# Kernel tuning notes

Measured on AMD Instinct MI355X. Metric: run time of the kernel, lower is better.

Reference implementation:

```python
import jax, jax.numpy as jnp
import numpy as np

B, L, D, H = 2, 4, 512, 8
HD = D // H
BLOCK, T_IDX, SEM = 2048, 2047, 50
NUM_VQ, CLIP = 1024, 512
T = T_IDX + 1  # condition token + idx tokens


def _ln(x, g, b):
    m = x.mean(-1, keepdims=True)
    v = ((x - m) ** 2).mean(-1, keepdims=True)
    return (x - m) * jax.lax.rsqrt(v + 1e-5) * g + b


def setup_inputs() -> dict:
    key = jax.random.key(0)
    ks = iter(jax.random.split(key, 48))
    p = lambda shape: 0.02 * jax.random.normal(next(ks), shape, jnp.float32)
    inp = {
        'idx': jax.random.randint(next(ks), (B, T_IDX), 0, NUM_VQ + 2, jnp.int32),
        'clip_feature': jax.random.normal(next(ks), (B, CLIP), jnp.float32),
        'tok_emb0': p((NUM_VQ + 2, D)),
        'tok_emb1': p((NUM_VQ + 2, D)),
        'cond_w': p((CLIP, D)), 'cond_b': jnp.zeros((D,), jnp.float32),
        'pos_emb': p((BLOCK, D)),
        'ln1_g': jnp.ones((L, D), jnp.float32), 'ln1_b': jnp.zeros((L, D), jnp.float32),
        'wq': p((L, D, D)), 'bq': jnp.zeros((L, D), jnp.float32),
        'wk': p((L, D, D)), 'bk': jnp.zeros((L, D), jnp.float32),
        'wv': p((L, D, D)), 'bv': jnp.zeros((L, D), jnp.float32),
        'wo': p((L, D, D)), 'bo': jnp.zeros((L, D), jnp.float32),
        'ln2_g': jnp.ones((L, D), jnp.float32), 'ln2_b': jnp.zeros((L, D), jnp.float32),
        'w1': p((L, D, 4 * D)), 'b1': jnp.zeros((L, 4 * D), jnp.float32),
        'w2': p((L, 4 * D, D)), 'b2': jnp.zeros((L, D), jnp.float32),
    }
    return inp


def reference(idx, clip_feature, tok_emb0, tok_emb1, cond_w, cond_b, pos_emb,
              ln1_g, ln1_b, wq, bq, wk, bk, wv, bv, wo, bo,
              ln2_g, ln2_b, w1, b1, w2, b2):
    # condition embedding + dual token embeddings (semantic / reconstruction split)
    cond = (clip_feature @ cond_w + cond_b)[:, None, :]          # [B,1,D]
    sem = tok_emb0[idx[:, :SEM]]                                  # [B,SEM,D]
    rec = tok_emb1[idx[:, SEM:]]                                  # [B,T_IDX-SEM,D]
    x = jnp.concatenate([cond, sem, rec], axis=1) + pos_emb[None, :T]  # [B,T,D]

    scale = 1.0 / np.sqrt(HD)
    causal = jnp.tril(jnp.ones((T, T), bool))                     # key <= query
    for i in range(L):
        h = _ln(x, ln1_g[i], ln1_b[i])
        q = (h @ wq[i] + bq[i]).reshape(B, T, H, HD)
        k = (h @ wk[i] + bk[i]).reshape(B, T, H, HD)
        v = (h @ wv[i] + bv[i]).reshape(B, T, H, HD)
        att = jnp.einsum('bthd,bshd->bhts', q, k) * scale        # [B,H,T,T]
        att = jnp.where(causal, att, -jnp.inf)
        att = jax.nn.softmax(att, axis=-1)
        y = jnp.einsum('bhts,bshd->bthd', att, v).reshape(B, T, D)
        x = x + y @ wo[i] + bo[i]
        h2 = _ln(x, ln2_g[i], ln2_b[i])
        x = x + jax.nn.gelu(h2 @ w1[i] + b1[i], approximate=False) @ w2[i] + b2[i]
    return x
```

## Files before the change

kernel.cpp:

```cpp
#include <hip/hip_runtime.h>
#include <math.h>

#define BB 2
#define TT 2048
#define DD 512
#define LL 4
#define HH 8
#define HDD 64
#define SEMN 50
#define CLIPN 512
#define NTOK (BB*TT)
#define QS 1024
#define VST 2056

typedef __bf16 bf16x8 __attribute__((ext_vector_type(8)));
typedef __bf16 bf16x4 __attribute__((ext_vector_type(4)));
typedef float  f32x4  __attribute__((ext_vector_type(4)));

#if __has_builtin(__builtin_amdgcn_global_load_lds)
#define USE_GLL 1
#endif

__device__ __forceinline__ void gll16(const __bf16* g, __bf16* l) {
#ifdef USE_GLL
  __builtin_amdgcn_global_load_lds((const __attribute__((address_space(1))) void*)g,
                                   (__attribute__((address_space(3))) void*)l, 16, 0, 0);
#endif
}

__device__ __forceinline__ float fexp2(float x) {
#if __has_builtin(__builtin_amdgcn_exp2f)
  return __builtin_amdgcn_exp2f(x);
#else
  return exp2f(x);
#endif
}

__global__ __launch_bounds__(128) void embed_kernel(
    const int* __restrict__ idx,
    const float* __restrict__ tok0, const float* __restrict__ tok1,
    const float* __restrict__ pos, float* __restrict__ x) {
  int row = blockIdx.x;
  int b = row / TT, t = row % TT;
  if (t == 0) return;
  int d4 = threadIdx.x << 2;
  int tok = idx[b*(TT-1) + (t-1)];
  const float* te = (t <= SEMN) ? tok0 : tok1;
  float4 e = *(const float4*)&te[(size_t)tok*DD + d4];
  float4 p = *(const float4*)&pos[(size_t)t*DD + d4];
  e.x += p.x; e.y += p.y; e.z += p.z; e.w += p.w;
  *(float4*)&x[(size_t)row*DD + d4] = e;
}

__global__ __launch_bounds__(256) void cond_kernel(
    const float* __restrict__ clip, const float* __restrict__ cw,
    const float* __restrict__ cb, const float* __restrict__ pos,
    float* __restrict__ x) {
  __shared__ float4 part[8][32];
  int b = blockIdx.x >> 2, dc = blockIdx.x & 3;
  int tid = threadIdx.x;
  int dv = tid & 31;
  int cg = tid >> 5;
  int d4 = dc*128 + dv*4;
  const float* cr = clip + b*CLIPN + cg*64;
  float4 acc = {0.f, 0.f, 0.f, 0.f};
  #pragma unroll 8
  for (int i = 0; i < 64; ++i) {
    float cv = cr[i];
    float4 w4 = *(const float4*)&cw[(size_t)(cg*64 + i)*DD + d4];
    acc.x = fmaf(cv, w4.x, acc.x); acc.y = fmaf(cv, w4.y, acc.y);
    acc.z = fmaf(cv, w4.z, acc.z); acc.w = fmaf(cv, w4.w, acc.w);
  }
  part[cg][dv] = acc;
  __syncthreads();
  if (tid < 32) {
    int dd4 = dc*128 + tid*4;
    float4 s = part[0][tid];
    #pragma unroll
    for (int g = 1; g < 8; ++g) {
      float4 q = part[g][tid];
      s.x += q.x; s.y += q.y; s.z += q.z; s.w += q.w;
    }
    float4 cbv = *(const float4*)&cb[dd4];
    float4 pv  = *(const float4*)&pos[dd4];
    s.x += cbv.x + pv.x; s.y += cbv.y + pv.y;
    s.z += cbv.z + pv.z; s.w += cbv.w + pv.w;
    *(float4*)&x[(size_t)(b*TT)*DD + dd4] = s;
  }
}

__global__ __launch_bounds__(256) void ln_kernel(const float* __restrict__ x,
                                                 const float* __restrict__ g,
                                                 const float* __restrict__ bta,
                                                 __bf16* __restrict__ out) {
  int l = threadIdx.x & 63;
  int row = blockIdx.x * 4 + (threadIdx.x >> 6);
  const float* xr = x + (size_t)row * DD + l*8;
  f32x4 a = *(const f32x4*)xr;
  f32x4 c = *(const f32x4*)(xr + 4);
  float s = a[0]+a[1]+a[2]+a[3]+c[0]+c[1]+c[2]+c[3];
  #pragma unroll
  for (int off = 1; off < 64; off <<= 1) s += __shfl_xor(s, off);
  float mean = s * (1.0f / DD);
  float d0 = a[0]-mean, d1 = a[1]-mean, d2 = a[2]-mean, d3 = a[3]-mean;
  float d4 = c[0]-mean, d5 = c[1]-mean, d6 = c[2]-mean, d7 = c[3]-mean;
  float sv = d0*d0+d1*d1+d2*d2+d3*d3+d4*d4+d5*d5+d6*d6+d7*d7;
  #pragma unroll
  for (int off = 1; off < 64; off <<= 1) sv += __shfl_xor(sv, off);
  float r = rsqrtf(sv * (1.0f / DD) + 1e-5f);
  f32x4 gv0 = *(const f32x4*)&g[l*8],   gv1 = *(const f32x4*)&g[l*8+4];
  f32x4 bv0 = *(const f32x4*)&bta[l*8], bv1 = *(const f32x4*)&bta[l*8+4];
  bf16x8 o;
  o[0] = (__bf16)(d0*r*gv0[0] + bv0[0]); o[1] = (__bf16)(d1*r*gv0[1] + bv0[1]);
  o[2] = (__bf16)(d2*r*gv0[2] + bv0[2]); o[3] = (__bf16)(d3*r*gv0[3] + bv0[3]);
  o[4] = (__bf16)(d4*r*gv1[0] + bv1[0]); o[5] = (__bf16)(d5*r*gv1[1] + bv1[1]);
  o[6] = (__bf16)(d6*r*gv1[2] + bv1[2]); o[7] = (__bf16)(d7*r*gv1[3] + bv1[3]);
  *(bf16x8*)&out[(size_t)row*DD + l*8] = o;
}

__global__ __launch_bounds__(256) void prep_kernel(
    const float* __restrict__ wq, const float* __restrict__ wk,
    const float* __restrict__ wv, const float* __restrict__ wo,
    const float* __restrict__ w1, const float* __restrict__ w2,
    __bf16* __restrict__ wbuf, size_t dstride) {
  __shared__ float tile[32][33];
  int id = blockIdx.x;
  int lay = blockIdx.y;
  size_t so4 = (size_t)lay * 262144, so16 = (size_t)lay * 1048576;
  __bf16* wb = wbuf + (size_t)lay * dstride;
  const float* src; __bf16* dst; int K, N, t;
  if (id < 1024) {
    int m = id >> 8; t = id & 255;
    src = ((m==0) ? wq : (m==1) ? wk : (m==2) ? wv : wo) + so4;
    dst = wb + (size_t)m * 262144; K = 512; N = 512;
  } else if (id < 2048) {
    t = id - 1024; src = w1 + so16; dst = wb + 1048576; K = 512; N = 2048;
  } else {
    t = id - 2048; src = w2 + so16; dst = wb + 2097152; K = 2048; N = 512;
  }
  int nsh = (N == 2048) ? 6 : 4;
  int tk = t >> nsh, tn = t & ((1 << nsh) - 1);
  int k0 = tk << 5, n0 = tn << 5;
  int tid = threadIdx.x;
  int r = tid >> 3, c = (tid & 7) << 2;
  float4 v = *(const float4*)&src[(size_t)(k0 + r)*N + n0 + c];
  tile[r][c+0] = v.x; tile[r][c+1] = v.y; tile[r][c+2] = v.z; tile[r][c+3] = v.w;
  __syncthreads();
  bf16x4 o;
  o[0] = (__bf16)tile[c+0][r];
  o[1] = (__bf16)tile[c+1][r];
  o[2] = (__bf16)tile[c+2][r];
  o[3] = (__bf16)tile[c+3][r];
  *(bf16x4*)&dst[(size_t)(n0 + r)*K + k0 + c] = o;
}

template<int TM, int TN, int QKV3, int RES, int GEL, int OB>
__global__ __launch_bounds__(256) void mgemm(
    const __bf16* __restrict__ A, const __bf16* __restrict__ Bt,
    const float* __restrict__ b0, const float* __restrict__ b1p, const float* __restrict__ b2p,
    const float* __restrict__ res, float* __restrict__ outF, __bf16* __restrict__ outB,
    __bf16* __restrict__ vtOut, int M, int N, int K, int ldo) {
  __shared__ __bf16 As[TM*64];
  __shared__ __bf16 Bs[TN*64];
  int tid = threadIdx.x, wave = tid >> 6, l = tid & 63;
  int l15 = l & 15, lg = l >> 4;
  int m0 = blockIdx.y * TM, n0 = blockIdx.x * TN;
  constexpr int WR = (TM == 128) ? 2 : 1;
  constexpr int WC = 4 / WR;
  constexpr int FM = TM / (16 * WR);
  constexpr int FN = TN / (16 * WC);
  int wr = wave / WC;
  int wc = wave % WC;

  f32x4 acc[FM][FN] = {};

  for (int k0 = 0; k0 < K; k0 += 64) {
#ifdef USE_GLL
    __syncthreads();
    #pragma unroll
    for (int g = wave; g < TM/8; g += 4) {
      int row = g*8 + (l >> 3);
      int lslot = (l & 7) ^ (row & 7);
      gll16(A + (size_t)(m0+row)*K + k0 + lslot*8, &As[g*512]);
    }
    #pragma unroll
    for (int g = wave; g < TN/8; g += 4) {
      int row = g*8 + (l >> 3);
      int lslot = (l & 7) ^ (row & 7);
      gll16(Bt + (size_t)(n0+row)*K + k0 + lslot*8, &Bs[g*512]);
    }
    asm volatile("s_waitcnt vmcnt(0)" ::: "memory");
    __syncthreads();
#else
    bf16x8 ar[TM/32], br[TN/32];
    #pragma unroll
    for (int c = 0; c < TM/32; ++c) {
      int idx = tid + c*256;
      int row = idx >> 3;
      int lslot = (idx & 7) ^ (row & 7);
      ar[c] = *(const bf16x8*)(A + (size_t)(m0+row)*K + k0 + lslot*8);
    }
    #pragma unroll
    for (int c = 0; c < TN/32; ++c) {
      int idx = tid + c*256;
      int row = idx >> 3;
      int lslot = (idx & 7) ^ (row & 7);
      br[c] = *(const bf16x8*)(Bt + (size_t)(n0+row)*K + k0 + lslot*8);
    }
    __syncthreads();
    #pragma unroll
    for (int c = 0; c < TM/32; ++c) {
      int idx = tid + c*256;
      *(bf16x8*)&As[(idx >> 3)*64 + (idx & 7)*8] = ar[c];
    }
    #pragma unroll
    for (int c = 0; c < TN/32; ++c) {
      int idx = tid + c*256;
      *(bf16x8*)&Bs[(idx >> 3)*64 + (idx & 7)*8] = br[c];
    }
    __syncthreads();
#endif
    bf16x8 af[FM][2], bfr[FN][2];
    #pragma unroll
    for (int mi = 0; mi < FM; ++mi) {
      int row = (wr*FM + mi)*16 + l15;
      #pragma unroll
      for (int h = 0; h < 2; ++h) {
        int ps = (h*4 + lg) ^ (row & 7);
        af[mi][h] = *(const bf16x8*)&As[row*64 + ps*8];
      }
    }
    #pragma unroll
    for (int ni = 0; ni < FN; ++ni) {
      int row = (wc*FN + ni)*16 + l15;
      #pragma unroll
      for (int h = 0; h < 2; ++h) {
        int ps = (h*4 + lg) ^ (row & 7);
        bfr[ni][h] = *(const bf16x8*)&Bs[row*64 + ps*8];
      }
    }
    #pragma unroll
    for (int mi = 0; mi < FM; ++mi)
      #pragma unroll
      for (int ni = 0; ni < FN; ++ni) {
        acc[mi][ni] = __builtin_amdgcn_mfma_f32_16x16x32_bf16(af[mi][0], bfr[ni][0], acc[mi][ni], 0, 0, 0);
        acc[mi][ni] = __builtin_amdgcn_mfma_f32_16x16x32_bf16(af[mi][1], bfr[ni][1], acc[mi][ni], 0, 0, 0);
      }
  }

  #pragma unroll
  for (int mi = 0; mi < FM; ++mi) {
    #pragma unroll
    for (int ni = 0; ni < FN; ++ni) {
      int col = n0 + (wc*FN + ni)*16 + l15;
      float bs;
      if (QKV3) bs = (col < 512) ? b0[col] : (col < 1024) ? b1p[col-512] : b2p[col-1024];
      else bs = b0[col];
      int row0 = m0 + (wr*FM + mi)*16 + (lg << 2);
      if (QKV3 && col >= 1024) {
        int hdg = col - 1024;
        bf16x4 pk;
        #pragma unroll
        for (int r = 0; r < 4; ++r) pk[r] = (__bf16)(acc[mi][ni][r] + bs);
        size_t vrow = (size_t)(((row0 >> 11)*8 + (hdg >> 6))*64 + (hdg & 63));
        *(bf16x4*)&vtOut[vrow*VST + (row0 & 2047)] = pk;
      } else {
        #pragma unroll
        for (int r = 0; r < 4; ++r) {
          int row = row0 + r;
          float v = acc[mi][ni][r] + bs;
          if (RES) v += res[(size_t)row*ldo + col];
          if (GEL) v = 0.5f * v * (1.0f + erff(v * 0.70710678118654752f));
          if (OB) outB[(size_t)row*ldo + col] = (__bf16)v;
          else    outF[(size_t)row*ldo + col] = v;
        }
      }
    }
  }
}

__global__ __launch_bounds__(256) void attn_kernel(const __bf16* __restrict__ qkv,
                                                   const __bf16* __restrict__ vt,
                                                   __bf16* __restrict__ y) {
  __shared__ float po[4][32][68];
  __shared__ float pmS[4][32];
  __shared__ float plS[4][4][32];
  int tid = threadIdx.x, wave = tid >> 6, l = tid & 63;
  int l15 = l & 15, lg = l >> 4;

  int wid = blockIdx.x;
  int g2 = 63 - (wid >> 4);
  int bh = wid & 15;
  int b = bh >> 3, h = bh & 7;
  int q0 = g2 * 32;

  const __bf16* qp = qkv + (size_t)(b*TT)*QS + h*HDD;
  const __bf16* kp = qp + 512;
  const __bf16* vtp = vt + ((size_t)bh*64 + l15)*VST + lg*8;
  const __bf16* kbase = kp + (size_t)l15*QS + lg*8;

  bf16x8 qf[2][2];
  {
    const float qs = 0.125f * 1.44269504088896f;
    #pragma unroll
    for (int f = 0; f < 2; ++f) {
      size_t qr = (size_t)(q0 + f*16 + l15) * QS + lg*8;
      bf16x8 t0 = *(const bf16x8*)(qp + qr);
      bf16x8 t1 = *(const bf16x8*)(qp + qr + 32);
      #pragma unroll
      for (int e = 0; e < 8; ++e) {
        qf[f][0][e] = (__bf16)((float)t0[e] * qs);
        qf[f][1][e] = (__bf16)((float)t1[e] * qs);
      }
    }
  }

  f32x4 o[2][4] = {};
  float m0 = 0.f, m1 = 0.f, ls0 = 0.f, ls1 = 0.f;
  int qpos0 = q0 + l15, qpos1 = q0 + 16 + l15;
  int nt = (q0 + 95) >> 6;
  int cs = (nt + 3) >> 2;
  int t0w = wave * cs;
  int t1w = t0w + cs; if (t1w > nt) t1w = nt;

  bf16x8 kf[4][2], vv[8];

#define KLOAD(KT) do {                                              \
    const __bf16* kr_ = kbase + (size_t)(KT)*64*QS;                 \
    _Pragma("unroll")                                               \
    for (int j_ = 0; j_ < 4; ++j_) {                                \
      kf[j_][0] = *(const bf16x8*)(kr_ + j_*16*QS);                 \
      kf[j_][1] = *(const bf16x8*)(kr_ + j_*16*QS + 32);            \
    }                                                               \
  } while (0)

#define VLOAD(KT) do {                                              \
    const __bf16* vr_ = vtp + (KT)*64;                              \
    _Pragma("unroll")                                               \
    for (int hc_ = 0; hc_ < 4; ++hc_) {                             \
      vv[hc_]     = *(const bf16x8*)(vr_ + hc_*16*VST);             \
      vv[hc_ + 4] = *(const bf16x8*)(vr_ + hc_*16*VST + 32);        \
    }                                                               \
  } while (0)

  if (t0w < t1w) {
    KLOAD(t0w);
    for (int kt = t0w; kt < t1w; ++kt) {
      VLOAD(kt);
      float sv[2][4][4];
      #pragma unroll
      for (int f = 0; f < 2; ++f)
        #pragma unroll
        for (int j = 0; j < 4; ++j) {
          f32x4 a_ = {};
          a_ = __builtin_amdgcn_mfma_f32_16x16x32_bf16(kf[j][0], qf[f][0], a_, 0, 0, 0);
          a_ = __builtin_amdgcn_mfma_f32_16x16x32_bf16(kf[j][1], qf[f][1], a_, 0, 0, 0);
          #pragma unroll
          for (int r = 0; r < 4; ++r) sv[f][j][r] = a_[r];
        }
      if (kt + 1 < t1w) KLOAD(kt + 1);
      if (kt == nt - 1) {
        #pragma unroll
        for (int j = 0; j < 4; ++j) {
          int kb0 = kt*64 + j*16 + lg*4;
          #pragma unroll
          for (int r = 0; r < 4; ++r) {
            if (kb0 + r > qpos0) sv[0][j][r] = -1e30f;
            if (kb0 + r > qpos1) sv[1][j][r] = -1e30f;
          }
        }
      }
      #pragma unroll
      for (int f = 0; f < 2; ++f) {
        float& m  = f ? m1 : m0;
        float& ls = f ? ls1 : ls0;
        float px = sv[f][0][0];
        #pragma unroll
        for (int j = 0; j < 4; ++j)
          #pragma unroll
          for (int r = 0; r < 4; ++r) px = fmaxf(px, sv[f][j][r]);
        if (!__all(px - m <= 8.0f)) {
          float u = px, w = px;
          asm("v_permlane32_swap_b32 %0, %1" : "+v"(u), "+v"(w));
          float t_ = fmaxf(u, w); u = t_; w = t_;
          asm("v_permlane16_swap_b32 %0, %1" : "+v"(u), "+v"(w));
          float tm = fmaxf(u, w);
          float mn = fmaxf(m, tm);
          float fc = fexp2(m - mn);
          m = mn; ls *= fc;
          float f0_ = __shfl(fc, lg*4+0), f1_ = __shfl(fc, lg*4+1);
          float f2_ = __shfl(fc, lg*4+2), f3_ = __shfl(fc, lg*4+3);
          #pragma unroll
          for (int hc = 0; hc < 4; ++hc) {
            o[f][hc][0] *= f0_; o[f][hc][1] *= f1_;
            o[f][hc][2] *= f2_; o[f][hc][3] *= f3_;
          }
        }
        float p_[4][4];
        float rs = 0.f;
        #pragma unroll
        for (int j = 0; j < 4; ++j)
          #pragma unroll
          for (int r = 0; r < 4; ++r) { p_[j][r] = fexp2(sv[f][j][r] - m); rs += p_[j][r]; }
        ls += rs;
        union PU { unsigned u[4]; bf16x8 v; };
        PU pa0, pa1;
        #pragma unroll
        for (int pair = 0; pair < 2; ++pair) {
          unsigned c0, c1, d0, d1;
          asm("v_cvt_pk_bf16_f32 %0, %1, %2" : "=v"(c0) : "v"(p_[2*pair][0]),   "v"(p_[2*pair][1]));
          asm("v_cvt_pk_bf16_f32 %0, %1, %2" : "=v"(c1) : "v"(p_[2*pair][2]),   "v"(p_[2*pair][3]));
          asm("v_cvt_pk_bf16_f32 %0, %1, %2" : "=v"(d0) : "v"(p_[2*pair+1][0]), "v"(p_[2*pair+1][1]));
          asm("v_cvt_pk_bf16_f32 %0, %1, %2" : "=v"(d1) : "v"(p_[2*pair+1][2]), "v"(p_[2*pair+1][3]));
          asm("v_permlane32_swap_b32 %0, %1" : "+v"(c0), "+v"(d0));
          asm("v_permlane32_swap_b32 %0, %1" : "+v"(c1), "+v"(d1));
          asm("v_permlane16_swap_b32 %0, %1" : "+v"(c0), "+v"(d0));
          asm("v_permlane16_swap_b32 %0, %1" : "+v"(c1), "+v"(d1));
          PU& pa = pair ? pa1 : pa0;
          pa.u[0] = c0; pa.u[1] = c1; pa.u[2] = d0; pa.u[3] = d1;
        }
        #pragma unroll
        for (int hc = 0; hc < 4; ++hc) {
          o[f][hc] = __builtin_amdgcn_mfma_f32_16x16x32_bf16(pa0.v, vv[hc],     o[f][hc], 0, 0, 0);
          o[f][hc] = __builtin_amdgcn_mfma_f32_16x16x32_bf16(pa1.v, vv[hc + 4], o[f][hc], 0, 0, 0);
        }
      }
    }
  }

  #pragma unroll
  for (int f = 0; f < 2; ++f)
    #pragma unroll
    for (int hc = 0; hc < 4; ++hc)
      #pragma unroll
      for (int r = 0; r < 4; ++r)
        po[wave][f*16 + lg*4 + r][hc*16 + l15] = o[f][hc][r];
  plS[wave][lg][l15]      = ls0;
  plS[wave][lg][16 + l15] = ls1;
  if (l < 16) { pmS[wave][l] = m0; pmS[wave][16 + l] = m1; }
  __syncthreads();

  #pragma unroll
  for (int rep = 0; rep < 2; ++rep) {
    int q = wave*4 + lg + rep*16;
    float e0 = pmS[0][q], e1 = pmS[1][q], e2 = pmS[2][q], e3 = pmS[3][q];
    float mstar = fmaxf(fmaxf(e0, e1), fmaxf(e2, e3));
    float f0 = fexp2(e0 - mstar), f1 = fexp2(e1 - mstar);
    float f2 = fexp2(e2 - mstar), f3 = fexp2(e3 - mstar);
    float l0 = plS[0][0][q] + plS[0][1][q] + plS[0][2][q] + plS[0][3][q];
    float l1 = plS[1][0][q] + plS[1][1][q] + plS[1][2][q] + plS[1][3][q];
    float l2 = plS[2][0][q] + plS[2][1][q] + plS[2][2][q] + plS[2][3][q];
    float l3 = plS[3][0][q] + plS[3][1][q] + plS[3][2][q] + plS[3][3][q];
    float lstar = l0*f0 + l1*f1 + l2*f2 + l3*f3;
    float inv = 1.0f / lstar;
    f32x4 o0 = *(const f32x4*)&po[0][q][l15*4];
    f32x4 o1 = *(const f32x4*)&po[1][q][l15*4];
    f32x4 o2 = *(const f32x4*)&po[2][q][l15*4];
    f32x4 o3 = *(const f32x4*)&po[3][q][l15*4];
    bf16x4 outv;
    #pragma unroll
    for (int j = 0; j < 4; ++j)
      outv[j] = (__bf16)((o0[j]*f0 + o1[j]*f1 + o2[j]*f2 + o3[j]*f3) * inv);
    size_t base = (size_t)(b*TT + q0 + q) * DD + h*HDD + l15*4;
    *(bf16x4*)&y[base] = outv;
  }
}

extern "C" void kernel_launch(void* const* d_in, const int* in_sizes, int n_in,
                              void* d_out, int out_size, void* d_ws, size_t ws_size,
                              hipStream_t stream) {
  const int*   idx    = (const int*)d_in[0];
  const float* clip   = (const float*)d_in[1];
  const float* tok0   = (const float*)d_in[2];
  const float* tok1   = (const float*)d_in[3];
  const float* cond_w = (const float*)d_in[4];
  const float* cond_b = (const float*)d_in[5];
  const float* pos    = (const float*)d_in[6];
  const float* ln1_g  = (const float*)d_in[7];
  const float* ln1_b  = (const float*)d_in[8];
  const float* wq     = (const float*)d_in[9];
  const float* bq     = (const float*)d_in[10];
  const float* wk     = (const float*)d_in[11];
  const float* bk     = (const float*)d_in[12];
  const float* wv     = (const float*)d_in[13];
  const float* bv     = (const float*)d_in[14];
  const float* wo     = (const float*)d_in[15];
  const float* bo     = (const float*)d_in[16];
  const float* ln2_g  = (const float*)d_in[17];
  const float* ln2_b  = (const float*)d_in[18];
  const float* w1     = (const float*)d_in[19];
  const float* b1     = (const float*)d_in[20];
  const float* w2     = (const float*)d_in[21];
  const float* b2     = (const float*)d_in[22];

  float* x = (float*)d_out;
  char* wsb = (char*)d_ws;
  bool bigws = ws_size >= 46153728ULL;

  __bf16* wbuf; __bf16* h; __bf16* qkv; __bf16* yb; __bf16* vt; __bf16* ffn;
  size_t wstride;
  if (bigws) {
    wbuf = (__bf16*)wsb;
    wstride = 3145728;
    h    = (__bf16*)(wsb + 25165824);
    qkv  = (__bf16*)(wsb + 29360128);
    yb   = (__bf16*)(wsb + 37748736);
    vt   = (__bf16*)(wsb + 41943040);
    ffn  = qkv;
  } else {
    wbuf = (__bf16*)wsb;
    wstride = 0;
    h    = (__bf16*)(wsb + 6291456);
    qkv  = (__bf16*)(wsb + 10485760);
    yb   = (__bf16*)(wsb + 23068672);
    vt   = (__bf16*)(wsb + 27262976);
    ffn  = qkv;
  }

  embed_kernel<<<dim3(NTOK), 128, 0, stream>>>(idx, tok0, tok1, pos, x);
  cond_kernel<<<dim3(8), 256, 0, stream>>>(clip, cond_w, cond_b, pos, x);

  if (bigws)
    prep_kernel<<<dim3(3072, LL), 256, 0, stream>>>(wq, wk, wv, wo, w1, w2, wbuf, wstride);

  for (int i = 0; i < LL; ++i) {
    __bf16* wb = wbuf + (size_t)i * wstride;
    if (!bigws)
      prep_kernel<<<dim3(3072, 1), 256, 0, stream>>>(
          wq + (size_t)i*262144, wk + (size_t)i*262144, wv + (size_t)i*262144,
          wo + (size_t)i*262144, w1 + (size_t)i*1048576, w2 + (size_t)i*1048576, wb, 0);

    ln_kernel<<<NTOK/4, 256, 0, stream>>>(x, ln1_g + i*DD, ln1_b + i*DD, h);

    mgemm<64,128,1,0,0,1><<<dim3(12, 64), 256, 0, stream>>>(
        h, wb, bq + i*DD, bk + i*DD, bv + i*DD, nullptr, nullptr, qkv, vt, NTOK, 1536, 512, 1024);

    attn_kernel<<<dim3(1024), 256, 0, stream>>>(qkv, vt, yb);

    mgemm<64,64,0,1,0,0><<<dim3(8, 64), 256, 0, stream>>>(
        yb, wb + 786432, bo + i*DD, nullptr, nullptr, x, x, nullptr, nullptr, NTOK, 512, 512, 512);

    ln_kernel<<<NTOK/4, 256, 0, stream>>>(x, ln2_g + i*DD, ln2_b + i*DD, h);

    mgemm<128,128,0,0,1,1><<<dim3(16, 32), 256, 0, stream>>>(
        h, wb + 1048576, b1 + (size_t)i*4*DD, nullptr, nullptr, nullptr, nullptr, ffn, nullptr, NTOK, 4*DD, 512, 2048);

    mgemm<64,64,0,1,0,0><<<dim3(8, 64), 256, 0, stream>>>(
        ffn, wb + 2097152, b2 + i*DD, nullptr, nullptr, x, x, nullptr, nullptr, NTOK, 512, 2048, 512);
  }
}
```

Baseline: 432.4 us.

## Double-buffer LDS tiles in mgemm to overlap global loads with MFMA

Turns the GEMM's single LDS buffer for the A and B tiles into two buffers. The next K-tile is prefetched with global_load_lds while MFMAs run on the current one, and a partial vmcnt wait plus raw barriers keep the stages in order. This targets the exposed global-memory latency of the old load-wait-compute loop. It doubles LDS use per block, which can lower occupancy. The wait counts are hardcoded per tile shape and must match the number of loads issued per stage.

```diff
diff --git a/kernel.cpp b/kernel.cpp
--- a/kernel.cpp
+++ b/kernel.cpp
@@ -160,8 +160,8 @@
     const float* __restrict__ b0, const float* __restrict__ b1p, const float* __restrict__ b2p,
     const float* __restrict__ res, float* __restrict__ outF, __bf16* __restrict__ outB,
     __bf16* __restrict__ vtOut, int M, int N, int K, int ldo) {
-  __shared__ __bf16 As[TM*64];
-  __shared__ __bf16 Bs[TN*64];
+  __shared__ __bf16 As[2][TM*64];
+  __shared__ __bf16 Bs[2][TN*64];
   int tid = threadIdx.x, wave = tid >> 6, l = tid & 63;
   int l15 = l & 15, lg = l >> 4;
   int m0 = blockIdx.y * TM, n0 = blockIdx.x * TN;
@@ -174,24 +174,72 @@
 
   f32x4 acc[FM][FN] = {};
 
-  for (int k0 = 0; k0 < K; k0 += 64) {
 #ifdef USE_GLL
-    __syncthreads();
+  constexpr int NL = TM/32 + TN/32;
+  auto stage = [&](int buf, int k0) {
     #pragma unroll
     for (int g = wave; g < TM/8; g += 4) {
       int row = g*8 + (l >> 3);
       int lslot = (l & 7) ^ (row & 7);
-      gll16(A + (size_t)(m0+row)*K + k0 + lslot*8, &As[g*512]);
+      gll16(A + (size_t)(m0+row)*K + k0 + lslot*8, &As[buf][g*512]);
     }
     #pragma unroll
     for (int g = wave; g < TN/8; g += 4) {
       int row = g*8 + (l >> 3);
       int lslot = (l & 7) ^ (row & 7);
-      gll16(Bt + (size_t)(n0+row)*K + k0 + lslot*8, &Bs[g*512]);
-    }
-    asm volatile("s_waitcnt vmcnt(0)" ::: "memory");
-    __syncthreads();
+      gll16(Bt + (size_t)(n0+row)*K + k0 + lslot*8, &Bs[buf][g*512]);
+    }
+  };
+  stage(0, 0);
+  int cur = 0;
+  for (int k0 = 0; k0 < K; k0 += 64) {
+    bool more = (k0 + 64 < K);
+    if (more) stage(cur ^ 1, k0 + 64);
+    if (more) {
+      if constexpr (NL == 4)      asm volatile("s_waitcnt vmcnt(4)" ::: "memory");
+      else if constexpr (NL == 6) asm volatile("s_waitcnt vmcnt(6)" ::: "memory");
+      else                        asm volatile("s_waitcnt vmcnt(8)" ::: "memory");
+    } else {
+      asm volatile("s_waitcnt vmcnt(0)" ::: "memory");
+    }
+    __builtin_amdgcn_s_barrier();
+    __builtin_amdgcn_sched_barrier(0);
+    const __bf16* Ac = As[cur];
+    const __bf16* Bc = Bs[cur];
+    bf16x8 af[FM][2], bfr[FN][2];
+    #pragma unroll
+    for (int mi = 0; mi < FM; ++mi) {
+      int row = (wr*FM + mi)*16 + l15;
+      #pragma unroll
+      for (int h = 0; h < 2; ++h) {
+        int ps = (h*4 + lg) ^ (row & 7);
+        af[mi][h] = *(const bf16x8*)&Ac[row*64 + ps*8];
+      }
+    }
+    #pragma unroll
+    for (int ni = 0; ni < FN; ++ni) {
+      int row = (wc*FN + ni)*16 + l15;
+      #pragma unroll
+      for (int h = 0; h < 2; ++h) {
+        int ps = (h*4 + lg) ^ (row & 7);
+        bfr[ni][h] = *(const bf16x8*)&Bc[row*64 + ps*8];
+      }
+    }
+    #pragma unroll
+    for (int mi = 0; mi < FM; ++mi)
+      #pragma unroll
+      for (int ni = 0; ni < FN; ++ni) {
+        acc[mi][ni] = __builtin_amdgcn_mfma_f32_16x16x32_bf16(af[mi][0], bfr[ni][0], acc[mi][ni], 0, 0, 0);
+        acc[mi][ni] = __builtin_amdgcn_mfma_f32_16x16x32_bf16(af[mi][1], bfr[ni][1], acc[mi][ni], 0, 0, 0);
+      }
+    if (more) {
+      __builtin_amdgcn_sched_barrier(0);
+      __builtin_amdgcn_s_barrier();
+    }
+    cur ^= 1;
+  }
 #else
+  for (int k0 = 0; k0 < K; k0 += 64) {
     bf16x8 ar[TM/32], br[TN/32];
     #pragma unroll
     for (int c = 0; c < TM/32; ++c) {
@@ -211,15 +259,14 @@
     #pragma unroll
     for (int c = 0; c < TM/32; ++c) {
       int idx = tid + c*256;
-      *(bf16x8*)&As[(idx >> 3)*64 + (idx & 7)*8] = ar[c];
+      *(bf16x8*)&As[0][(idx >> 3)*64 + (idx & 7)*8] = ar[c];
     }
     #pragma unroll
     for (int c = 0; c < TN/32; ++c) {
       int idx = tid + c*256;
-      *(bf16x8*)&Bs[(idx >> 3)*64 + (idx & 7)*8] = br[c];
+      *(bf16x8*)&Bs[0][(idx >> 3)*64 + (idx & 7)*8] = br[c];
     }
     __syncthreads();
-#endif
     bf16x8 af[FM][2], bfr[FN][2];
     #pragma unroll
     for (int mi = 0; mi < FM; ++mi) {
@@ -227,7 +274,7 @@
       #pragma unroll
       for (int h = 0; h < 2; ++h) {
         int ps = (h*4 + lg) ^ (row & 7);
-        af[mi][h] = *(const bf16x8*)&As[row*64 + ps*8];
+        af[mi][h] = *(const bf16x8*)&As[0][row*64 + ps*8];
       }
     }
     #pragma unroll
@@ -236,7 +283,7 @@
       #pragma unroll
       for (int h = 0; h < 2; ++h) {
         int ps = (h*4 + lg) ^ (row & 7);
-        bfr[ni][h] = *(const bf16x8*)&Bs[row*64 + ps*8];
+        bfr[ni][h] = *(const bf16x8*)&Bs[0][row*64 + ps*8];
       }
     }
     #pragma unroll
@@ -246,7 +293,9 @@
         acc[mi][ni] = __builtin_amdgcn_mfma_f32_16x16x32_bf16(af[mi][0], bfr[ni][0], acc[mi][ni], 0, 0, 0);
         acc[mi][ni] = __builtin_amdgcn_mfma_f32_16x16x32_bf16(af[mi][1], bfr[ni][1], acc[mi][ni], 0, 0, 0);
       }
-  }
+    __syncthreads();
+  }
+#endif
 
   #pragma unroll
   for (int mi = 0; mi < FM; ++mi) {
```

Result: no change. 439.0 us (+1.5%).

## Fuse LayerNorm into QKV and FFN1 GEMM A-tile loads

Applied to the files above, without the earlier changes.

Removes the standalone LayerNorm kernels. The QKV and FFN-up GEMMs now read fp32 residual rows directly, compute per-row mean and rstd in a prologue using a one-pass sum/sum-of-squares, and normalize and convert to bf16 while filling the swizzled A tile. The FFN-up GEMM tile also changes from 128x128 to 64x128, and the FFN buffer moves to the freed h slot. This saves launches and the bf16 h round-trip, but each N-tile block now recomputes row statistics and normalization. The A loads become synchronous fp32 reads instead of async LDS copies, and one-pass variance is slightly less accurate.

```diff
diff --git a/kernel.cpp b/kernel.cpp
--- a/kernel.cpp
+++ b/kernel.cpp
@@ -87,35 +87,6 @@
     s.z += cbv.z + pv.z; s.w += cbv.w + pv.w;
     *(float4*)&x[(size_t)(b*TT)*DD + dd4] = s;
   }
-}
-
-__global__ __launch_bounds__(256) void ln_kernel(const float* __restrict__ x,
-                                                 const float* __restrict__ g,
-                                                 const float* __restrict__ bta,
-                                                 __bf16* __restrict__ out) {
-  int l = threadIdx.x & 63;
-  int row = blockIdx.x * 4 + (threadIdx.x >> 6);
-  const float* xr = x + (size_t)row * DD + l*8;
-  f32x4 a = *(const f32x4*)xr;
-  f32x4 c = *(const f32x4*)(xr + 4);
-  float s = a[0]+a[1]+a[2]+a[3]+c[0]+c[1]+c[2]+c[3];
-  #pragma unroll
-  for (int off = 1; off < 64; off <<= 1) s += __shfl_xor(s, off);
-  float mean = s * (1.0f / DD);
-  float d0 = a[0]-mean, d1 = a[1]-mean, d2 = a[2]-mean, d3 = a[3]-mean;
-  float d4 = c[0]-mean, d5 = c[1]-mean, d6 = c[2]-mean, d7 = c[3]-mean;
-  float sv = d0*d0+d1*d1+d2*d2+d3*d3+d4*d4+d5*d5+d6*d6+d7*d7;
-  #pragma unroll
-  for (int off = 1; off < 64; off <<= 1) sv += __shfl_xor(sv, off);
-  float r = rsqrtf(sv * (1.0f / DD) + 1e-5f);
-  f32x4 gv0 = *(const f32x4*)&g[l*8],   gv1 = *(const f32x4*)&g[l*8+4];
-  f32x4 bv0 = *(const f32x4*)&bta[l*8], bv1 = *(const f32x4*)&bta[l*8+4];
-  bf16x8 o;
-  o[0] = (__bf16)(d0*r*gv0[0] + bv0[0]); o[1] = (__bf16)(d1*r*gv0[1] + bv0[1]);
-  o[2] = (__bf16)(d2*r*gv0[2] + bv0[2]); o[3] = (__bf16)(d3*r*gv0[3] + bv0[3]);
-  o[4] = (__bf16)(d4*r*gv1[0] + bv1[0]); o[5] = (__bf16)(d5*r*gv1[1] + bv1[1]);
-  o[6] = (__bf16)(d6*r*gv1[2] + bv1[2]); o[7] = (__bf16)(d7*r*gv1[3] + bv1[3]);
-  *(bf16x8*)&out[(size_t)row*DD + l*8] = o;
 }
 
 __global__ __launch_bounds__(256) void prep_kernel(
@@ -154,14 +125,18 @@
   *(bf16x4*)&dst[(size_t)(n0 + r)*K + k0 + c] = o;
 }
 
-template<int TM, int TN, int QKV3, int RES, int GEL, int OB>
+template<int TM, int TN, int FLN, int QKV3, int RES, int GEL, int OB>
 __global__ __launch_bounds__(256) void mgemm(
-    const __bf16* __restrict__ A, const __bf16* __restrict__ Bt,
+    const __bf16* __restrict__ A, const float* __restrict__ Af,
+    const float* __restrict__ lng, const float* __restrict__ lnb,
+    const __bf16* __restrict__ Bt,
     const float* __restrict__ b0, const float* __restrict__ b1p, const float* __restrict__ b2p,
     const float* __restrict__ res, float* __restrict__ outF, __bf16* __restrict__ outB,
     __bf16* __restrict__ vtOut, int M, int N, int K, int ldo) {
   __shared__ __bf16 As[TM*64];
   __shared__ __bf16 Bs[TN*64];
+  __shared__ float ps[FLN ? TM : 1][4][2];
+  __shared__ float rowm[FLN ? TM : 1], rowr[FLN ? TM : 1];
   int tid = threadIdx.x, wave = tid >> 6, l = tid & 63;
   int l15 = l & 15, lg = l >> 4;
   int m0 = blockIdx.y * TM, n0 = blockIdx.x * TN;
@@ -174,14 +149,75 @@
 
   f32x4 acc[FM][FN] = {};
 
+  if (FLN) {
+    int r = tid >> 2, qd = tid & 3;
+    const float* xr = Af + (size_t)(m0 + r)*DD + qd*128;
+    float s = 0.f, s2 = 0.f;
+    #pragma unroll 8
+    for (int i = 0; i < 32; ++i) {
+      float4 v = *(const float4*)(xr + i*4);
+      s  += v.x + v.y + v.z + v.w;
+      s2 += v.x*v.x + v.y*v.y + v.z*v.z + v.w*v.w;
+    }
+    ps[r][qd][0] = s; ps[r][qd][1] = s2;
+    __syncthreads();
+    if (tid < TM) {
+      float ss  = ps[tid][0][0] + ps[tid][1][0] + ps[tid][2][0] + ps[tid][3][0];
+      float ss2 = ps[tid][0][1] + ps[tid][1][1] + ps[tid][2][1] + ps[tid][3][1];
+      float mean = ss * (1.0f / DD);
+      float var  = ss2 * (1.0f / DD) - mean*mean;
+      rowm[tid] = mean;
+      rowr[tid] = rsqrtf(var + 1e-5f);
+    }
+  }
+
   for (int k0 = 0; k0 < K; k0 += 64) {
+    __syncthreads();
+    if (FLN) {
+      int row = tid >> 2;
+      int sl = (tid & 3) << 1;
+      const float* src = Af + (size_t)(m0 + row)*DD + k0 + sl*8;
+      float mean = rowm[row], rstd = rowr[row];
+      float4 v0 = *(const float4*)(src);
+      float4 v1 = *(const float4*)(src + 4);
+      float4 v2 = *(const float4*)(src + 8);
+      float4 v3 = *(const float4*)(src + 12);
+      float4 g0 = *(const float4*)&lng[k0 + sl*8];
+      float4 g1 = *(const float4*)&lng[k0 + sl*8 + 4];
+      float4 g2 = *(const float4*)&lng[k0 + sl*8 + 8];
+      float4 g3 = *(const float4*)&lng[k0 + sl*8 + 12];
+      float4 be0 = *(const float4*)&lnb[k0 + sl*8];
+      float4 be1 = *(const float4*)&lnb[k0 + sl*8 + 4];
+      float4 be2 = *(const float4*)&lnb[k0 + sl*8 + 8];
+      float4 be3 = *(const float4*)&lnb[k0 + sl*8 + 12];
+      bf16x8 o0, o1;
+      o0[0] = (__bf16)((v0.x-mean)*rstd*g0.x + be0.x);
+      o0[1] = (__bf16)((v0.y-mean)*rstd*g0.y + be0.y);
+      o0[2] = (__bf16)((v0.z-mean)*rstd*g0.z + be0.z);
+      o0[3] = (__bf16)((v0.w-mean)*rstd*g0.w + be0.w);
+      o0[4] = (__bf16)((v1.x-mean)*rstd*g1.x + be1.x);
+      o0[5] = (__bf16)((v1.y-mean)*rstd*g1.y + be1.y);
+      o0[6] = (__bf16)((v1.z-mean)*rstd*g1.z + be1.z);
+      o0[7] = (__bf16)((v1.w-mean)*rstd*g1.w + be1.w);
+      o1[0] = (__bf16)((v2.x-mean)*rstd*g2.x + be2.x);
+      o1[1] = (__bf16)((v2.y-mean)*rstd*g2.y + be2.y);
+      o1[2] = (__bf16)((v2.z-mean)*rstd*g2.z + be2.z);
+      o1[3] = (__bf16)((v2.w-mean)*rstd*g2.w + be2.w);
+      o1[4] = (__bf16)((v3.x-mean)*rstd*g3.x + be3.x);
+      o1[5] = (__bf16)((v3.y-mean)*rstd*g3.y + be3.y);
+      o1[6] = (__bf16)((v3.z-mean)*rstd*g3.z + be3.z);
+      o1[7] = (__bf16)((v3.w-mean)*rstd*g3.w + be3.w);
+      *(bf16x8*)&As[row*64 + ((sl+0) ^ (row & 7))*8] = o0;
+      *(bf16x8*)&As[row*64 + ((sl+1) ^ (row & 7))*8] = o1;
+    }
 #ifdef USE_GLL
-    __syncthreads();
-    #pragma unroll
-    for (int g = wave; g < TM/8; g += 4) {
-      int row = g*8 + (l >> 3);
-      int lslot = (l & 7) ^ (row & 7);
-      gll16(A + (size_t)(m0+row)*K + k0 + lslot*8, &As[g*512]);
+    if (!FLN) {
+      #pragma unroll
+      for (int g = wave; g < TM/8; g += 4) {
+        int row = g*8 + (l >> 3);
+        int lslot = (l & 7) ^ (row & 7);
+        gll16(A + (size_t)(m0+row)*K + k0 + lslot*8, &As[g*512]);
+      }
     }
     #pragma unroll
     for (int g = wave; g < TN/8; g += 4) {
@@ -192,33 +228,39 @@
     asm volatile("s_waitcnt vmcnt(0)" ::: "memory");
     __syncthreads();
 #else
-    bf16x8 ar[TM/32], br[TN/32];
-    #pragma unroll
-    for (int c = 0; c < TM/32; ++c) {
-      int idx = tid + c*256;
-      int row = idx >> 3;
-      int lslot = (idx & 7) ^ (row & 7);
-      ar[c] = *(const bf16x8*)(A + (size_t)(m0+row)*K + k0 + lslot*8);
-    }
-    #pragma unroll
-    for (int c = 0; c < TN/32; ++c) {
-      int idx = tid + c*256;
-      int row = idx >> 3;
-      int lslot = (idx & 7) ^ (row & 7);
-      br[c] = *(const bf16x8*)(Bt + (size_t)(n0+row)*K + k0 + lslot*8);
-    }
-    __syncthreads();
-    #pragma unroll
-    for (int c = 0; c < TM/32; ++c) {
-      int idx = tid + c*256;
-      *(bf16x8*)&As[(idx >> 3)*64 + (idx & 7)*8] = ar[c];
-    }
-    #pragma unroll
-    for (int c = 0; c < TN/32; ++c) {
-      int idx = tid + c*256;
-      *(bf16x8*)&Bs[(idx >> 3)*64 + (idx & 7)*8] = br[c];
-    }
-    __syncthreads();
+    {
+      bf16x8 br[TN/32];
+      #pragma unroll
+      for (int c = 0; c < TN/32; ++c) {
+        int idx = tid + c*256;
+        int row = idx >> 3;
+        int lslot = (idx & 7) ^ (row & 7);
+        br[c] = *(const bf16x8*)(Bt + (size_t)(n0+row)*K + k0 + lslot*8);
+      }
+      bf16x8 ar[TM/32];
+      if (!FLN) {
+        #pragma unroll
+        for (int c = 0; c < TM/32; ++c) {
+          int idx = tid + c*256;
+          int row = idx >> 3;
+          int lslot = (idx & 7) ^ (row & 7);
+          ar[c] = *(const bf16x8*)(A + (size_t)(m0+row)*K + k0 + lslot*8);
+        }
+      }
+      #pragma unroll
+      for (int c = 0; c < TN/32; ++c) {
+        int idx = tid + c*256;
+        *(bf16x8*)&Bs[(idx >> 3)*64 + (idx & 7)*8] = br[c];
+      }
+      if (!FLN) {
+        #pragma unroll
+        for (int c = 0; c < TM/32; ++c) {
+          int idx = tid + c*256;
+          *(bf16x8*)&As[(idx >> 3)*64 + (idx & 7)*8] = ar[c];
+        }
+      }
+      __syncthreads();
+    }
 #endif
     bf16x8 af[FM][2], bfr[FN][2];
     #pragma unroll
@@ -226,8 +268,8 @@
       int row = (wr*FM + mi)*16 + l15;
       #pragma unroll
       for (int h = 0; h < 2; ++h) {
-        int ps = (h*4 + lg) ^ (row & 7);
-        af[mi][h] = *(const bf16x8*)&As[row*64 + ps*8];
+        int psl = (h*4 + lg) ^ (row & 7);
+        af[mi][h] = *(const bf16x8*)&As[row*64 + psl*8];
       }
     }
     #pragma unroll
@@ -235,8 +277,8 @@
       int row = (wc*FN + ni)*16 + l15;
       #pragma unroll
       for (int h = 0; h < 2; ++h) {
-        int ps = (h*4 + lg) ^ (row & 7);
-        bfr[ni][h] = *(const bf16x8*)&Bs[row*64 + ps*8];
+        int psl = (h*4 + lg) ^ (row & 7);
+        bfr[ni][h] = *(const bf16x8*)&Bs[row*64 + psl*8];
       }
     }
     #pragma unroll
@@ -497,24 +539,22 @@
   char* wsb = (char*)d_ws;
   bool bigws = ws_size >= 46153728ULL;
 
-  __bf16* wbuf; __bf16* h; __bf16* qkv; __bf16* yb; __bf16* vt; __bf16* ffn;
+  __bf16* wbuf; __bf16* qkv; __bf16* yb; __bf16* vt; __bf16* ffn;
   size_t wstride;
   if (bigws) {
     wbuf = (__bf16*)wsb;
     wstride = 3145728;
-    h    = (__bf16*)(wsb + 25165824);
     qkv  = (__bf16*)(wsb + 29360128);
     yb   = (__bf16*)(wsb + 37748736);
     vt   = (__bf16*)(wsb + 41943040);
-    ffn  = qkv;
+    ffn  = (__bf16*)(wsb + 25165824);
   } else {
     wbuf = (__bf16*)wsb;
     wstride = 0;
-    h    = (__bf16*)(wsb + 6291456);
     qkv  = (__bf16*)(wsb + 10485760);
     yb   = (__bf16*)(wsb + 23068672);
     vt   = (__bf16*)(wsb + 27262976);
-    ffn  = qkv;
+    ffn  = (__bf16*)(wsb + 6291456);
   }
 
   embed_kernel<<<dim3(NTOK), 128, 0, stream>>>(idx, tok0, tok1, pos, x);
@@ -530,22 +570,22 @@
           wq + (size_t)i*262144, wk + (size_t)i*262144, wv + (size_t)i*262144,
           wo + (size_t)i*262144, w1 + (size_t)i*1048576, w2 + (size_t)i*1048576, wb, 0);
 
-    ln_kernel<<<NTOK/4, 256, 0, stream>>>(x, ln1_g + i*DD, ln1_b + i*DD, h);
-
-    mgemm<64,128,1,0,0,1><<<dim3(12, 64), 256, 0, stream>>>(
-        h, wb, bq + i*DD, bk + i*DD, bv + i*DD, nullptr, nullptr, qkv, vt, NTOK, 1536, 512, 1024);
+    mgemm<64,128,1,1,0,0,1><<<dim3(12, 64), 256, 0, stream>>>(
+        nullptr, x, ln1_g + i*DD, ln1_b + i*DD, wb,
+        bq + i*DD, bk + i*DD, bv + i*DD, nullptr, nullptr, qkv, vt, NTOK, 1536, 512, 1024);
 
     attn_kernel<<<dim3(1024), 256, 0, stream>>>(qkv, vt, yb);
 
-    mgemm<64,64,0,1,0,0><<<dim3(8, 64), 256, 0, stream>>>(
-        yb, wb + 786432, bo + i*DD, nullptr, nullptr, x, x, nullptr, nullptr, NTOK, 512, 512, 512);
-
-    ln_kernel<<<NTOK/4, 256, 0, stream>>>(x, ln2_g + i*DD, ln2_b + i*DD, h);
-
-    mgemm<128,128,0,0,1,1><<<dim3(16, 32), 256, 0, stream>>>(
-        h, wb + 1048576, b1 + (size_t)i*4*DD, nullptr, nullptr, nullptr, nullptr, ffn, nullptr, NTOK, 4*DD, 512, 2048);
-
-    mgemm<64,64,0,1,0,0><<<dim3(8, 64), 256, 0, stream>>>(
-        ffn, wb + 2097152, b2 + i*DD, nullptr, nullptr, x, x, nullptr, nullptr, NTOK, 512, 2048, 512);
-  }
-}
+    mgemm<64,64,0,0,1,0,0><<<dim3(8, 64), 256, 0, stream>>>(
+        yb, nullptr, nullptr, nullptr, wb + 786432,
+        bo + i*DD, nullptr, nullptr, x, x, nullptr, nullptr, NTOK, 512, 512, 512);
+
+    mgemm<64,128,1,0,0,1,1><<<dim3(16, 64), 256, 0, stream>>>(
+        nullptr, x, ln2_g + i*DD, ln2_b + i*DD, wb + 1048576,
+        b1 + (size_t)i*4*DD, nullptr, nullptr, nullptr, nullptr, ffn, nullptr, NTOK, 4*DD, 512, 2048);
+
+    mgemm<64,64,0,0,1,0,0><<<dim3(8, 64), 256, 0, stream>>>(
+        ffn, nullptr, nullptr, nullptr, wb + 2097152,
+        b2 + i*DD, nullptr, nullptr, x, x, nullptr, nullptr, NTOK, 512, 2048, 512);
+  }
+}
```

After: 635.1 us. +46.9%, slower.
